# Performance work log

Measured on AMD Instinct MI355X. Metric: run time of the kernel, lower is better.

Reference implementation:

```python
import jax, jax.numpy as jnp
import numpy as np

NV, NJ, NB_POSE = 778, 16, 135
PARENTS = np.array([-1, 0, 1, 2, 0, 4, 5, 0, 7, 8, 0, 10, 11, 0, 13, 14], dtype=np.int32)
FINGER_IDX = np.array([734, 333, 443, 555, 678], dtype=np.int32)


def setup_inputs() -> dict:
    key = jax.random.key(0)
    ks = jax.random.split(key, 9)
    B = 4096
    return {
        "beta": jax.random.normal(ks[0], (B, 10), jnp.float32) * 0.3,
        "theta": jax.random.normal(ks[1], (B, 48), jnp.float32) * 0.3,
        "v_template": jax.random.normal(ks[2], (NV, 3), jnp.float32) * 0.05,
        "shapedirs": jax.random.normal(ks[3], (10, NV * 3), jnp.float32) * 0.01,
        "posedirs": jax.random.normal(ks[4], (NB_POSE, NV * 3), jnp.float32) * 0.01,
        "J_regressor": jax.random.uniform(ks[5], (NV, NJ), jnp.float32) / NV,
        "weights": jax.random.uniform(ks[6], (NV, NJ), jnp.float32),
        "hands_mean": jax.random.normal(ks[7], (45,), jnp.float32) * 0.1,
        "hands_components": jax.random.normal(ks[8], (45, 45), jnp.float32) * 0.1,
    }


def batch_rodrigues(r):
    """Axis-angle [N,3] -> rotation matrices [N,3,3] (Rodrigues formula)."""
    eps = 1e-8
    angle = jnp.linalg.norm(r + eps, axis=1, keepdims=True)          # [N,1]
    axis = r / angle
    x, y, z = axis[:, 0], axis[:, 1], axis[:, 2]
    zeros = jnp.zeros_like(x)
    K = jnp.stack([zeros, -z, y, z, zeros, -x, -y, x, zeros], axis=1).reshape(-1, 3, 3)
    a = angle[:, :, None]                                            # [N,1,1]
    I3 = jnp.eye(3, dtype=r.dtype)
    return I3 + jnp.sin(a) * K + (1.0 - jnp.cos(a)) * (K @ K)


def global_rigid_transform(Rs, Js):
    """Rs [B,16,3,3], Js [B,16,3] -> relative skinning transforms A [B,16,4,4]."""
    B = Rs.shape[0]
    bot = jnp.broadcast_to(jnp.array([0.0, 0.0, 0.0, 1.0], Rs.dtype), (B, 1, 4))

    def make_A(R, t):  # R [B,3,3], t [B,3] -> [B,4,4]
        return jnp.concatenate([jnp.concatenate([R, t[:, :, None]], axis=2), bot], axis=1)

    results = [make_A(Rs[:, 0], Js[:, 0])]
    for i in range(1, NJ):  # fixed small kinematic chain
        t = Js[:, i] - Js[:, PARENTS[i]]
        results.append(results[PARENTS[i]] @ make_A(Rs[:, i], t))
    res = jnp.stack(results, axis=1)                                 # [B,16,4,4]
    Js_h = jnp.concatenate([Js, jnp.zeros((B, NJ, 1), Rs.dtype)], axis=2)  # [B,16,4]
    init_bone = jnp.einsum('bjpq,bjq->bjp', res, Js_h)               # [B,16,4]
    return res.at[:, :, :, 3].add(-init_bone)                        # A = res - pack(res @ [J;0])


def reference(beta, theta, v_template, shapedirs, posedirs, J_regressor, weights,
              hands_mean, hands_components):
    B = beta.shape[0]
    P = theta.shape[1] - 3
    # full pose: global rot + PCA-recovered local rotations
    full_local = theta[:, 3:] @ hands_components[:P, :] + hands_mean  # [B,45]
    pose = jnp.concatenate([theta[:, :3], full_local], axis=1)       # [B,48]

    # shape blend
    v_shaped = (beta @ shapedirs).reshape(B, NV, 3) + v_template     # [B,778,3]
    J = jnp.einsum('bvc,vj->bjc', v_shaped, J_regressor)             # [B,16,3]

    # pose blend
    Rs = batch_rodrigues(pose.reshape(-1, 3)).reshape(B, NJ, 3, 3)
    pose_feature = (Rs[:, 1:] - jnp.eye(3, dtype=Rs.dtype)).reshape(B, NB_POSE)
    v_posed = (pose_feature @ posedirs).reshape(B, NV, 3) + v_shaped

    # kinematic chain + linear blend skinning
    A = global_rigid_transform(Rs, J)                                # [B,16,4,4]
    T = jnp.einsum('vj,bjpq->bvpq', weights, A)                      # [B,778,4,4]
    v_homo = jnp.concatenate([v_posed, jnp.ones((B, NV, 1), v_posed.dtype)], axis=2)
    verts = jnp.einsum('bvpq,bvq->bvp', T, v_homo)[:, :, :3]         # [B,778,3]

    joints = jnp.einsum('bvc,vj->bjc', verts, J_regressor)           # [B,16,3]
    joints = jnp.concatenate([joints, verts[:, FINGER_IDX, :]], axis=1)  # [B,21,3]
    return joints
```

## Files before the change

### kernel.cpp

```cpp
#include <hip/hip_runtime.h>

#define NV  778
#define NBP 135
#define NK  146
#define NKQ 152
#define GC  8
#define VCH 49

#define FV0 734
#define FV1 333
#define FV2 443
#define FV3 555
#define FV4 678

__device__ __forceinline__ const float* d_row(int k,
                                              const float* vt,
                                              const float* sd,
                                              const float* pd) {
    return (k == 0) ? vt : (k <= 10 ? sd + (size_t)(k-1)*(NV*3)
                                    : pd + (size_t)(k-11)*(NV*3));
}

__launch_bounds__(256)
__global__ void k_fold(const float* __restrict__ vt,
                       const float* __restrict__ sd,
                       const float* __restrict__ pd,
                       const float* __restrict__ jreg,
                       const float* __restrict__ wts,
                       const float* __restrict__ beta,
                       const float* __restrict__ theta,
                       const float* __restrict__ hm,
                       const float* __restrict__ hc,
                       float* __restrict__ SJ, float* __restrict__ JT,
                       float* __restrict__ WJ, float* __restrict__ Gq,
                       float* __restrict__ coefG, float* __restrict__ R0G,
                       float* __restrict__ Dfing, float* __restrict__ Wfing,
                       int Btot, int npb)
{
    const int o = blockIdx.x;
    const int tid = threadIdx.x;

    __shared__ float p_hc[2025];
    __shared__ float p_th[8][48];
    __shared__ float p_pose[8][45];
    __shared__ float l_j[VCH*16];
    __shared__ float l_w[VCH*16];
    __shared__ float l_d[VCH*3];

    if (o < 2336) {
        const int k = o >> 4, chunk = o & 15;
        const float* Drow = d_row(k, vt, sd, pd);
        const int v0 = chunk * VCH;
        const int v1 = (v0 + VCH < NV) ? (v0 + VCH) : NV;
        const int n = v1 - v0;
        for (int i = tid; i < n*16; i += 256) l_j[i] = jreg[v0*16 + i];
        for (int i = tid; i < n*16; i += 256) l_w[i] = wts[v0*16 + i];
        for (int i = tid; i < n*3;  i += 256) l_d[i] = Drow[v0*3 + i];
        __syncthreads();
        const int J = tid >> 4, j = tid & 15;
        float a0 = 0.f, a1 = 0.f, a2 = 0.f;
        #pragma unroll 7
        for (int v = 0; v < n; ++v) {
            float pv = l_j[v*16 + J] * l_w[v*16 + j];
            a0 += l_d[v*3+0] * pv;
            a1 += l_d[v*3+1] * pv;
            a2 += l_d[v*3+2] * pv;
        }
        float* gp = Gq + ((size_t)k*256 + tid)*3;
        atomicAdd(gp+0, a0);
        atomicAdd(gp+1, a1);
        atomicAdd(gp+2, a2);
    } else if (o < 2468) {
        const int idx = (o - 2336)*4 + (tid >> 6);
        const int t = tid & 63;
        const float* src; int jc;
        if (idx < 480) { int k = idx / 48; jc = idx % 48; src = sd + (size_t)k*(NV*3); }
        else           { jc = idx - 480;              src = vt; }
        int j = jc / 3, c = jc % 3;
        float acc = 0.f;
        for (int v = t; v < NV; v += 64)
            acc += src[3*v + c] * jreg[v*16 + j];
        for (int off = 32; off; off >>= 1) acc += __shfl_down(acc, off, 64);
        if (t == 0) { if (idx < 480) SJ[idx] = acc; else JT[jc] = acc; }
    } else if (o < 2532) {
        const int cidx = (o - 2468)*4 + (tid >> 6);
        const int t = tid & 63;
        const int J = cidx >> 4, j = cidx & 15;
        float acc = 0.f;
        for (int v = t; v < NV; v += 64)
            acc += jreg[v*16 + J] * wts[v*16 + j];
        for (int off = 32; off; off >>= 1) acc += __shfl_down(acc, off, 64);
        if (t == 0) WJ[cidx] = acc;
    } else if (o < 2532 + npb) {
        const int b0 = (o - 2532) * 8;
        for (int i = tid; i < 2025; i += 256) p_hc[i] = hc[i];
        for (int i = tid; i < 8*48; i += 256) {
            int g = i / 48, t = i % 48, b = b0 + g;
            p_th[g][t] = (b < Btot) ? theta[(size_t)b*48 + t] : 0.f;
        }
        __syncthreads();
        for (int i = tid; i < 8*45; i += 256) {
            int g = i / 45, t = i % 45;
            float acc = hm[t];
            #pragma unroll 9
            for (int k = 0; k < 45; ++k) acc += p_th[g][3+k] * p_hc[k*45 + t];
            p_pose[g][t] = acc;
        }
        __syncthreads();
        if (tid < 128) {
            int g = tid >> 4, jt = tid & 15;
            int b = b0 + g;
            if (b < Btot) {
                float rx, ry, rz;
                if (jt == 0) { rx = p_th[g][0]; ry = p_th[g][1]; rz = p_th[g][2]; }
                else { rx = p_pose[g][3*(jt-1)+0]; ry = p_pose[g][3*(jt-1)+1]; rz = p_pose[g][3*(jt-1)+2]; }
                float ex = rx + 1e-8f, ey = ry + 1e-8f, ez = rz + 1e-8f;
                float angle = sqrtf(ex*ex + ey*ey + ez*ez);
                float inv = 1.f / angle;
                float x = rx*inv, y = ry*inv, z = rz*inv;
                float s  = sinf(angle);
                float c1 = 1.f - cosf(angle);
                float R[9];
                R[0] = 1.f + c1*(-(z*z + y*y));
                R[1] = -s*z + c1*(x*y);
                R[2] =  s*y + c1*(x*z);
                R[3] =  s*z + c1*(x*y);
                R[4] = 1.f + c1*(-(x*x + z*z));
                R[5] = -s*x + c1*(y*z);
                R[6] = -s*y + c1*(x*z);
                R[7] =  s*x + c1*(y*z);
                R[8] = 1.f + c1*(-(x*x + y*y));
                float* cg = coefG + (size_t)b*152;
                if (jt == 0) {
                    #pragma unroll
                    for (int i = 0; i < 9; ++i) R0G[(size_t)b*9 + i] = R[i];
                    cg[0] = 1.f;
                    #pragma unroll
                    for (int k = 0; k < 10; ++k) cg[1+k] = beta[(size_t)b*10 + k];
                    #pragma unroll
                    for (int k = 146; k < 152; ++k) cg[k] = 0.f;
                } else {
                    #pragma unroll
                    for (int i = 0; i < 9; ++i)
                        cg[11 + (jt-1)*9 + i] = R[i] - ((i % 4 == 0) ? 1.f : 0.f);
                }
            }
        }
    } else {
        const int fv[5] = {FV0, FV1, FV2, FV3, FV4};
        for (int e = tid; e < NK*15; e += 256) {
            int k = e / 15, r = e % 15, f = r / 3, q = r % 3;
            Dfing[e] = d_row(k, vt, sd, pd)[3*fv[f] + q];
        }
        if (tid < 80) {
            int f = tid >> 4, j = tid & 15;
            Wfing[tid] = wts[fv[f]*16 + j];
        }
    }
}

__launch_bounds__(256)
__global__ void kC(const float* __restrict__ SJ,
                   const float* __restrict__ JT,
                   const float* __restrict__ WJ,
                   const float* __restrict__ Gq,
                   const float* __restrict__ coefG,
                   const float* __restrict__ R0G,
                   const float* __restrict__ Dfing,
                   const float* __restrict__ Wfing,
                   float* __restrict__ out,
                   int Btot)
{
    const int tid = threadIdx.x;
    const int w = tid >> 6, t = tid & 63;
    const int b0 = blockIdx.x * GC;

    __shared__ float s_SJ[480];
    __shared__ float s_JT[48];
    __shared__ float s_WJ[256];
    __shared__ __align__(16) float s_coef[GC][152];
    __shared__ float s_R0[GC][9];
    __shared__ float s_A[GC][192];
    __shared__ float s_J[GC][48];
    __shared__ float s_vpf[GC][16];
    __shared__ float s_fred[GC][15][2];

    float cur0[8], cur1[8], cur2[8];
    #pragma unroll
    for (int kk = 0; kk < 8; ++kk) {
        const float* gq = Gq + ((size_t)kk*256 + tid)*3;
        cur0[kk] = gq[0]; cur1[kk] = gq[1]; cur2[kk] = gq[2];
    }

    for (int i = tid; i < 480; i += 256) s_SJ[i] = SJ[i];
    if (tid < 48) s_JT[tid] = JT[tid];
    s_WJ[tid] = WJ[tid];
    for (int i = tid; i < GC*152; i += 256) {
        int g = i / 152, k = i % 152, b = b0 + g;
        s_coef[g][k] = (b < Btot) ? coefG[(size_t)b*152 + k] : 0.f;
    }
    if (tid < GC*9) {
        int g = tid / 9, i = tid % 9, b = b0 + g;
        s_R0[g][i] = (b < Btot) ? R0G[(size_t)b*9 + i] : 0.f;
    }
    __syncthreads();

    #pragma unroll
    for (int pp = 0; pp < 2; ++pp) {
        const int g = pp*4 + w;
        const int b = b0 + g;
        if (b < Btot) {
            if (t < 48) {
                float acc = s_JT[t];
                #pragma unroll
                for (int k = 0; k < 10; ++k) acc += s_coef[g][1+k] * s_SJ[k*48 + t];
                s_J[g][t] = acc;
            }
            if (t < 16) {
                float* Jg = s_J[g];
                float res[12];
                #pragma unroll
                for (int p = 0; p < 3; ++p) {
                    res[p*4+0] = s_R0[g][p*3+0];
                    res[p*4+1] = s_R0[g][p*3+1];
                    res[p*4+2] = s_R0[g][p*3+2];
                    res[p*4+3] = Jg[p];
                }
                if (t >= 1) {
                    int start = ((t-1)/3)*3 + 1;
                    int d = t - start;
                    for (int s = 0; s < 3; ++s) {
                        if (s <= d) {
                            int a  = start + s;
                            int pa = (s == 0) ? 0 : (a - 1);
                            const float* cr = &s_coef[g][11 + (a-1)*9];
                            float Ra[9];
                            #pragma unroll
                            for (int i = 0; i < 9; ++i)
                                Ra[i] = cr[i] + ((i % 4 == 0) ? 1.f : 0.f);
                            float ax = Jg[a*3+0] - Jg[pa*3+0];
                            float ay = Jg[a*3+1] - Jg[pa*3+1];
                            float az = Jg[a*3+2] - Jg[pa*3+2];
                            float nr[12];
                            #pragma unroll
                            for (int p = 0; p < 3; ++p) {
                                float r0 = res[p*4+0], r1 = res[p*4+1], r2 = res[p*4+2];
                                #pragma unroll
                                for (int q = 0; q < 3; ++q)
                                    nr[p*4+q] = r0*Ra[q] + r1*Ra[3+q] + r2*Ra[6+q];
                                nr[p*4+3] = r0*ax + r1*ay + r2*az + res[p*4+3];
                            }
                            #pragma unroll
                            for (int q = 0; q < 12; ++q) res[q] = nr[q];
                        }
                    }
                }
                float jx = Jg[t*3+0], jy = Jg[t*3+1], jz = Jg[t*3+2];
                #pragma unroll
                for (int p = 0; p < 3; ++p) {
                    float r0 = res[p*4+0], r1 = res[p*4+1], r2 = res[p*4+2];
                    float ib = r0*jx + r1*jy + r2*jz;
                    s_A[g][t*12 + p*4+0] = r0;
                    s_A[g][t*12 + p*4+1] = r1;
                    s_A[g][t*12 + p*4+2] = r2;
                    s_A[g][t*12 + p*4+3] = res[p*4+3] - ib;
                }
            }
        }
    }
    __syncthreads();

    float acc[GC][3];
    #pragma unroll
    for (int g = 0; g < GC; ++g) { acc[g][0]=0.f; acc[g][1]=0.f; acc[g][2]=0.f; }
    for (int k = 0; k < NKQ; k += 8) {
        float nxt0[8], nxt1[8], nxt2[8];
        if (k + 8 < NKQ) {
            #pragma unroll
            for (int kk = 0; kk < 8; ++kk) {
                const float* gq = Gq + ((size_t)(k+8+kk)*256 + tid)*3;
                nxt0[kk] = gq[0]; nxt1[kk] = gq[1]; nxt2[kk] = gq[2];
            }
        }
        #pragma unroll
        for (int g = 0; g < GC; ++g) {
            float4 cA = *(const float4*)&s_coef[g][k];
            float4 cB = *(const float4*)&s_coef[g][k+4];
            float cf[8] = {cA.x,cA.y,cA.z,cA.w, cB.x,cB.y,cB.z,cB.w};
            #pragma unroll
            for (int kk = 0; kk < 8; ++kk) {
                acc[g][0] += cf[kk]*cur0[kk];
                acc[g][1] += cf[kk]*cur1[kk];
                acc[g][2] += cf[kk]*cur2[kk];
            }
        }
        if (k + 8 < NKQ) {
            #pragma unroll
            for (int kk = 0; kk < 8; ++kk) {
                cur0[kk] = nxt0[kk]; cur1[kk] = nxt1[kk]; cur2[kk] = nxt2[kk];
            }
        }
    }

    {
        const int J = tid >> 4, j = tid & 15;
        #pragma unroll
        for (int g = 0; g < GC; ++g) {
            const float* Aj = &s_A[g][j*12];
            float wj = s_WJ[J*16 + j];
            float v0 = Aj[0]*acc[g][0] + Aj[1]*acc[g][1] + Aj[2]*acc[g][2]  + Aj[3]*wj;
            float v1 = Aj[4]*acc[g][0] + Aj[5]*acc[g][1] + Aj[6]*acc[g][2]  + Aj[7]*wj;
            float v2 = Aj[8]*acc[g][0] + Aj[9]*acc[g][1] + Aj[10]*acc[g][2] + Aj[11]*wj;
            #pragma unroll
            for (int off = 1; off < 16; off <<= 1) {
                v0 += __shfl_xor(v0, off, 64);
                v1 += __shfl_xor(v1, off, 64);
                v2 += __shfl_xor(v2, off, 64);
            }
            int b = b0 + g;
            if (j == 0 && b < Btot) {
                float* ob = out + (size_t)b*63 + J*3;
                ob[0] = v0; ob[1] = v1; ob[2] = v2;
            }
        }
    }

    if (tid < GC*30) {
        int g = tid / 30, rem = tid % 30, sl = rem / 15, r = rem % 15;
        int k0 = sl*73, k1 = (k0+73 < NK) ? k0+73 : NK;
        float a = 0.f;
        for (int k = k0; k < k1; ++k) a += s_coef[g][k] * Dfing[k*15 + r];
        s_fred[g][r][sl] = a;
    }
    __syncthreads();
    if (tid < GC*15) {
        int g = tid / 15, r = tid % 15;
        s_vpf[g][r] = s_fred[g][r][0] + s_fred[g][r][1];
    }
    __syncthreads();
    if (tid < GC*15) {
        int g = tid / 15, r = tid % 15, f = r / 3, p = r % 3;
        int b = b0 + g;
        if (b < Btot) {
            const float* Ag = s_A[g];
            float vx = s_vpf[g][f*3+0], vy = s_vpf[g][f*3+1], vz = s_vpf[g][f*3+2];
            float val = 0.f;
            #pragma unroll
            for (int j = 0; j < 16; ++j) {
                float wj = Wfing[f*16 + j];
                val += wj * (Ag[j*12 + p*4 + 0]*vx +
                             Ag[j*12 + p*4 + 1]*vy +
                             Ag[j*12 + p*4 + 2]*vz +
                             Ag[j*12 + p*4 + 3]);
            }
            out[(size_t)b*63 + (16+f)*3 + p] = val;
        }
    }
}

extern "C" void kernel_launch(void* const* d_in, const int* in_sizes, int n_in,
                              void* d_out, int out_size, void* d_ws, size_t ws_size,
                              hipStream_t stream) {
    const float* beta       = (const float*)d_in[0];
    const float* theta      = (const float*)d_in[1];
    const float* v_template = (const float*)d_in[2];
    const float* shapedirs  = (const float*)d_in[3];
    const float* posedirs   = (const float*)d_in[4];
    const float* J_reg      = (const float*)d_in[5];
    const float* weights    = (const float*)d_in[6];
    const float* hands_mean = (const float*)d_in[7];
    const float* hands_comp = (const float*)d_in[8];
    float* out = (float*)d_out;

    const int B = in_sizes[0] / 10;
    const int npb = (B + 7) / 8;

    float* W = (float*)d_ws;
    float* SJ    = W;
    float* JT    = W + 480;
    float* WJ    = W + 528;
    float* Dfing = W + 784;
    float* Wfing = W + 2974;
    float* Gq    = W + 3072;
    float* coefG = W + 119808;
    float* R0G   = coefG + (size_t)B*152;

    hipMemsetAsync(Gq, 0, (size_t)NKQ*768*sizeof(float), stream);
    k_fold<<<2533 + npb, 256, 0, stream>>>(v_template, shapedirs, posedirs, J_reg,
                                           weights, beta, theta, hands_mean, hands_comp,
                                           SJ, JT, WJ, Gq, coefG, R0G, Dfing, Wfing,
                                           B, npb);
    kC<<<(B + GC - 1)/GC, 256, 0, stream>>>(SJ, JT, WJ, Gq, coefG, R0G,
                                            Dfing, Wfing, out, B);
}
```

Measured before the change: 125.9 us.

## Fuse memset and both kernels into one cooperative kernel with grid syncs

Replaces the memset plus the two kernel launches with a single cooperative kernel. Grid-wide barriers separate three phases: zeroing Gq and computing per-batch pose coefficients, the folding reductions distributed over blocks, and the final per-batch skinning. This removes launch and inter-kernel gaps. In exchange, each block now runs several folding work units one after another instead of one per block, and the kernel must keep all blocks resident at once for the cooperative launch.

Result: slower. 264.0 us (+109.7%).

```diff
diff --git a/kernel.cpp b/kernel.cpp
--- a/kernel.cpp
+++ b/kernel.cpp
@@ -1,11 +1,14 @@
 #include <hip/hip_runtime.h>
+#include <hip/hip_cooperative_groups.h>
+
+namespace cg = cooperative_groups;
 
 #define NV  778
-#define NBP 135
 #define NK  146
 #define NKQ 152
 #define GC  8
 #define VCH 49
+#define NU  2533
 
 #define FV0 734
 #define FV1 333
@@ -22,23 +25,27 @@
 }
 
 __launch_bounds__(256)
-__global__ void k_fold(const float* __restrict__ vt,
-                       const float* __restrict__ sd,
-                       const float* __restrict__ pd,
-                       const float* __restrict__ jreg,
-                       const float* __restrict__ wts,
-                       const float* __restrict__ beta,
-                       const float* __restrict__ theta,
-                       const float* __restrict__ hm,
-                       const float* __restrict__ hc,
-                       float* __restrict__ SJ, float* __restrict__ JT,
-                       float* __restrict__ WJ, float* __restrict__ Gq,
-                       float* __restrict__ coefG, float* __restrict__ R0G,
-                       float* __restrict__ Dfing, float* __restrict__ Wfing,
-                       int Btot, int npb)
+__global__ void k_all(const float* __restrict__ vt,
+                      const float* __restrict__ sd,
+                      const float* __restrict__ pd,
+                      const float* __restrict__ jreg,
+                      const float* __restrict__ wts,
+                      const float* __restrict__ beta,
+                      const float* __restrict__ theta,
+                      const float* __restrict__ hm,
+                      const float* __restrict__ hc,
+                      float* __restrict__ SJ, float* __restrict__ JT,
+                      float* __restrict__ WJ, float* __restrict__ Gq,
+                      float* __restrict__ coefG, float* __restrict__ R0G,
+                      float* __restrict__ Dfing, float* __restrict__ Wfing,
+                      float* __restrict__ out,
+                      int Btot)
 {
-    const int o = blockIdx.x;
-    const int tid = threadIdx.x;
+    cg::grid_group grid = cg::this_grid();
+    const int tid  = threadIdx.x;
+    const int blk  = blockIdx.x;
+    const int nblk = gridDim.x;
+    const int w = tid >> 6, t = tid & 63;
 
     __shared__ float p_hc[2025];
     __shared__ float p_th[8][48];
@@ -46,65 +53,32 @@
     __shared__ float l_j[VCH*16];
     __shared__ float l_w[VCH*16];
     __shared__ float l_d[VCH*3];
-
-    if (o < 2336) {
-        const int k = o >> 4, chunk = o & 15;
-        const float* Drow = d_row(k, vt, sd, pd);
-        const int v0 = chunk * VCH;
-        const int v1 = (v0 + VCH < NV) ? (v0 + VCH) : NV;
-        const int n = v1 - v0;
-        for (int i = tid; i < n*16; i += 256) l_j[i] = jreg[v0*16 + i];
-        for (int i = tid; i < n*16; i += 256) l_w[i] = wts[v0*16 + i];
-        for (int i = tid; i < n*3;  i += 256) l_d[i] = Drow[v0*3 + i];
-        __syncthreads();
-        const int J = tid >> 4, j = tid & 15;
-        float a0 = 0.f, a1 = 0.f, a2 = 0.f;
-        #pragma unroll 7
-        for (int v = 0; v < n; ++v) {
-            float pv = l_j[v*16 + J] * l_w[v*16 + j];
-            a0 += l_d[v*3+0] * pv;
-            a1 += l_d[v*3+1] * pv;
-            a2 += l_d[v*3+2] * pv;
-        }
-        float* gp = Gq + ((size_t)k*256 + tid)*3;
-        atomicAdd(gp+0, a0);
-        atomicAdd(gp+1, a1);
-        atomicAdd(gp+2, a2);
-    } else if (o < 2468) {
-        const int idx = (o - 2336)*4 + (tid >> 6);
-        const int t = tid & 63;
-        const float* src; int jc;
-        if (idx < 480) { int k = idx / 48; jc = idx % 48; src = sd + (size_t)k*(NV*3); }
-        else           { jc = idx - 480;              src = vt; }
-        int j = jc / 3, c = jc % 3;
-        float acc = 0.f;
-        for (int v = t; v < NV; v += 64)
-            acc += src[3*v + c] * jreg[v*16 + j];
-        for (int off = 32; off; off >>= 1) acc += __shfl_down(acc, off, 64);
-        if (t == 0) { if (idx < 480) SJ[idx] = acc; else JT[jc] = acc; }
-    } else if (o < 2532) {
-        const int cidx = (o - 2468)*4 + (tid >> 6);
-        const int t = tid & 63;
-        const int J = cidx >> 4, j = cidx & 15;
-        float acc = 0.f;
-        for (int v = t; v < NV; v += 64)
-            acc += jreg[v*16 + J] * wts[v*16 + j];
-        for (int off = 32; off; off >>= 1) acc += __shfl_down(acc, off, 64);
-        if (t == 0) WJ[cidx] = acc;
-    } else if (o < 2532 + npb) {
-        const int b0 = (o - 2532) * 8;
+    __shared__ float s_SJ[480];
+    __shared__ float s_JT[48];
+    __shared__ float s_WJ[256];
+    __shared__ __align__(16) float s_coef[GC][152];
+    __shared__ float s_R0[GC][9];
+    __shared__ float s_A[GC][192];
+    __shared__ float s_J[GC][48];
+    __shared__ float s_vpf[GC][16];
+    __shared__ float s_fred[GC][15][2];
+
+    for (int i = blk*256 + tid; i < NKQ*768; i += nblk*256) Gq[i] = 0.f;
+
+    {
+        const int b0 = blk * 8;
         for (int i = tid; i < 2025; i += 256) p_hc[i] = hc[i];
         for (int i = tid; i < 8*48; i += 256) {
-            int g = i / 48, t = i % 48, b = b0 + g;
-            p_th[g][t] = (b < Btot) ? theta[(size_t)b*48 + t] : 0.f;
+            int g = i / 48, tt = i % 48, b = b0 + g;
+            p_th[g][tt] = (b < Btot) ? theta[(size_t)b*48 + tt] : 0.f;
         }
         __syncthreads();
         for (int i = tid; i < 8*45; i += 256) {
-            int g = i / 45, t = i % 45;
-            float acc = hm[t];
+            int g = i / 45, tt = i % 45;
+            float acc = hm[tt];
             #pragma unroll 9
-            for (int k = 0; k < 45; ++k) acc += p_th[g][3+k] * p_hc[k*45 + t];
-            p_pose[g][t] = acc;
+            for (int k = 0; k < 45; ++k) acc += p_th[g][3+k] * p_hc[k*45 + tt];
+            p_pose[g][tt] = acc;
         }
         __syncthreads();
         if (tid < 128) {
@@ -130,60 +104,88 @@
                 R[6] = -s*y + c1*(x*z);
                 R[7] =  s*x + c1*(y*z);
                 R[8] = 1.f + c1*(-(x*x + y*y));
-                float* cg = coefG + (size_t)b*152;
+                float* cg_ = coefG + (size_t)b*152;
                 if (jt == 0) {
                     #pragma unroll
                     for (int i = 0; i < 9; ++i) R0G[(size_t)b*9 + i] = R[i];
-                    cg[0] = 1.f;
+                    cg_[0] = 1.f;
                     #pragma unroll
-                    for (int k = 0; k < 10; ++k) cg[1+k] = beta[(size_t)b*10 + k];
+                    for (int k = 0; k < 10; ++k) cg_[1+k] = beta[(size_t)b*10 + k];
                     #pragma unroll
-                    for (int k = 146; k < 152; ++k) cg[k] = 0.f;
+                    for (int k = 146; k < 152; ++k) cg_[k] = 0.f;
                 } else {
                     #pragma unroll
                     for (int i = 0; i < 9; ++i)
-                        cg[11 + (jt-1)*9 + i] = R[i] - ((i % 4 == 0) ? 1.f : 0.f);
+                        cg_[11 + (jt-1)*9 + i] = R[i] - ((i % 4 == 0) ? 1.f : 0.f);
                 }
             }
         }
-    } else {
-        const int fv[5] = {FV0, FV1, FV2, FV3, FV4};
-        for (int e = tid; e < NK*15; e += 256) {
-            int k = e / 15, r = e % 15, f = r / 3, q = r % 3;
-            Dfing[e] = d_row(k, vt, sd, pd)[3*fv[f] + q];
-        }
-        if (tid < 80) {
-            int f = tid >> 4, j = tid & 15;
-            Wfing[tid] = wts[fv[f]*16 + j];
-        }
-    }
-}
-
-__launch_bounds__(256)
-__global__ void kC(const float* __restrict__ SJ,
-                   const float* __restrict__ JT,
-                   const float* __restrict__ WJ,
-                   const float* __restrict__ Gq,
-                   const float* __restrict__ coefG,
-                   const float* __restrict__ R0G,
-                   const float* __restrict__ Dfing,
-                   const float* __restrict__ Wfing,
-                   float* __restrict__ out,
-                   int Btot)
-{
-    const int tid = threadIdx.x;
-    const int w = tid >> 6, t = tid & 63;
-    const int b0 = blockIdx.x * GC;
-
-    __shared__ float s_SJ[480];
-    __shared__ float s_JT[48];
-    __shared__ float s_WJ[256];
-    __shared__ __align__(16) float s_coef[GC][152];
-    __shared__ float s_R0[GC][9];
-    __shared__ float s_A[GC][192];
-    __shared__ float s_J[GC][48];
-    __shared__ float s_vpf[GC][16];
-    __shared__ float s_fred[GC][15][2];
+    }
+    grid.sync();
+
+    const int upb = (NU + nblk - 1) / nblk;
+    for (int i = 0; i < upb; ++i) {
+        const int u = blk*upb + i;
+        if (u < 2336) {
+            const int k = u >> 4, chunk = u & 15;
+            const float* Drow = d_row(k, vt, sd, pd);
+            const int v0 = chunk * VCH;
+            const int v1 = (v0 + VCH < NV) ? (v0 + VCH) : NV;
+            const int n = v1 - v0;
+            __syncthreads();
+            for (int e = tid; e < n*16; e += 256) l_j[e] = jreg[v0*16 + e];
+            for (int e = tid; e < n*16; e += 256) l_w[e] = wts[v0*16 + e];
+            for (int e = tid; e < n*3;  e += 256) l_d[e] = Drow[v0*3 + e];
+            __syncthreads();
+            const int J = tid >> 4, j = tid & 15;
+            float a0 = 0.f, a1 = 0.f, a2 = 0.f;
+            #pragma unroll 7
+            for (int v = 0; v < n; ++v) {
+                float pv = l_j[v*16 + J] * l_w[v*16 + j];
+                a0 += l_d[v*3+0] * pv;
+                a1 += l_d[v*3+1] * pv;
+                a2 += l_d[v*3+2] * pv;
+            }
+            float* gp = Gq + ((size_t)k*256 + tid)*3;
+            atomicAdd(gp+0, a0);
+            atomicAdd(gp+1, a1);
+            atomicAdd(gp+2, a2);
+        } else if (u < 2468) {
+            const int idx = (u - 2336)*4 + (tid >> 6);
+            const int tt = tid & 63;
+            const float* src; int jc;
+            if (idx < 480) { int k = idx / 48; jc = idx % 48; src = sd + (size_t)k*(NV*3); }
+            else           { jc = idx - 480;              src = vt; }
+            int j = jc / 3, c = jc % 3;
+            float acc = 0.f;
+            for (int v = tt; v < NV; v += 64)
+                acc += src[3*v + c] * jreg[v*16 + j];
+            for (int off = 32; off; off >>= 1) acc += __shfl_down(acc, off, 64);
+            if (tt == 0) { if (idx < 480) SJ[idx] = acc; else JT[jc] = acc; }
+        } else if (u < 2532) {
+            const int cidx = (u - 2468)*4 + (tid >> 6);
+            const int tt = tid & 63;
+            const int J = cidx >> 4, j = cidx & 15;
+            float acc = 0.f;
+            for (int v = tt; v < NV; v += 64)
+                acc += jreg[v*16 + J] * wts[v*16 + j];
+            for (int off = 32; off; off >>= 1) acc += __shfl_down(acc, off, 64);
+            if (tt == 0) WJ[cidx] = acc;
+        } else if (u == 2532) {
+            const int fv[5] = {FV0, FV1, FV2, FV3, FV4};
+            for (int e = tid; e < NK*15; e += 256) {
+                int k = e / 15, r = e % 15, f = r / 3, q = r % 3;
+                Dfing[e] = d_row(k, vt, sd, pd)[3*fv[f] + q];
+            }
+            if (tid < 80) {
+                int f = tid >> 4, j = tid & 15;
+                Wfing[tid] = wts[fv[f]*16 + j];
+            }
+        }
+    }
+    grid.sync();
+
+    const int b0 = blk * GC;
 
     float cur0[8], cur1[8], cur2[8];
     #pragma unroll
@@ -200,8 +202,8 @@
         s_coef[g][k] = (b < Btot) ? coefG[(size_t)b*152 + k] : 0.f;
     }
     if (tid < GC*9) {
-        int g = tid / 9, i = tid % 9, b = b0 + g;
-        s_R0[g][i] = (b < Btot) ? R0G[(size_t)b*9 + i] : 0.f;
+        int g = tid / 9, i2 = tid % 9, b = b0 + g;
+        s_R0[g][i2] = (b < Btot) ? R0G[(size_t)b*9 + i2] : 0.f;
     }
     __syncthreads();
 
@@ -236,8 +238,8 @@
                             const float* cr = &s_coef[g][11 + (a-1)*9];
                             float Ra[9];
                             #pragma unroll
-                            for (int i = 0; i < 9; ++i)
-                                Ra[i] = cr[i] + ((i % 4 == 0) ? 1.f : 0.f);
+                            for (int i2 = 0; i2 < 9; ++i2)
+                                Ra[i2] = cr[i2] + ((i2 % 4 == 0) ? 1.f : 0.f);
                             float ax = Jg[a*3+0] - Jg[pa*3+0];
                             float ay = Jg[a*3+1] - Jg[pa*3+1];
                             float az = Jg[a*3+2] - Jg[pa*3+2];
@@ -373,7 +375,7 @@
     float* out = (float*)d_out;
 
     const int B = in_sizes[0] / 10;
-    const int npb = (B + 7) / 8;
+    const int nblk = (B + GC - 1) / GC;
 
     float* W = (float*)d_ws;
     float* SJ    = W;
@@ -385,11 +387,14 @@
     float* coefG = W + 119808;
     float* R0G   = coefG + (size_t)B*152;
 
-    hipMemsetAsync(Gq, 0, (size_t)NKQ*768*sizeof(float), stream);
-    k_fold<<<2533 + npb, 256, 0, stream>>>(v_template, shapedirs, posedirs, J_reg,
-                                           weights, beta, theta, hands_mean, hands_comp,
-                                           SJ, JT, WJ, Gq, coefG, R0G, Dfing, Wfing,
-                                           B, npb);
-    kC<<<(B + GC - 1)/GC, 256, 0, stream>>>(SJ, JT, WJ, Gq, coefG, R0G,
-                                            Dfing, Wfing, out, B);
+    void* args[] = {
+        (void*)&v_template, (void*)&shapedirs, (void*)&posedirs,
+        (void*)&J_reg, (void*)&weights,
+        (void*)&beta, (void*)&theta, (void*)&hands_mean, (void*)&hands_comp,
+        (void*)&SJ, (void*)&JT, (void*)&WJ, (void*)&Gq,
+        (void*)&coefG, (void*)&R0G, (void*)&Dfing, (void*)&Wfing,
+        (void*)&out, (void*)&B
+    };
+    hipLaunchCooperativeKernel((const void*)k_all, dim3(nblk), dim3(256),
+                               args, 0, stream);
 }
```
